# Performance work log

Measured on AMD Instinct MI355X. Metric: run time of the kernel, lower is better.

## Reference

```python
import jax, jax.numpy as jnp
import numpy as np

LN_EPS = 1e-5


def setup_inputs() -> dict:
    key = jax.random.key(0)
    ks = jax.random.split(key, 5)
    N, E, D = 50000, 600000, 128
    x = jax.random.normal(ks[0], (N, D), dtype=jnp.float32)
    edge_index = jax.random.randint(ks[1], (2, E), 0, N, dtype=jnp.int64)
    W_l = jax.random.normal(ks[2], (D, D), dtype=jnp.float32) * (1.0 / np.sqrt(D))
    b_l = jnp.zeros((D,), dtype=jnp.float32)
    W_r = jax.random.normal(ks[3], (D, D), dtype=jnp.float32) * (1.0 / np.sqrt(D))
    gamma = jnp.ones((D,), dtype=jnp.float32)
    beta = jnp.zeros((D,), dtype=jnp.float32)
    return {"x": x, "edge_index": edge_index, "W_l": W_l, "b_l": b_l,
            "W_r": W_r, "gamma": gamma, "beta": beta}


def reference(x, edge_index, W_l, b_l, W_r, gamma, beta):
    # SAGEConv (mean aggregation): out = lin_l(mean_{j in N(i)} x_j) + lin_r(x_i)
    N = x.shape[0]
    src, dst = edge_index[0], edge_index[1]
    msg = x[src]                                                # (E, D) gather
    agg = jax.ops.segment_sum(msg, dst, num_segments=N)         # (N, D) scatter-add
    cnt = jax.ops.segment_sum(jnp.ones_like(dst, dtype=x.dtype), dst, num_segments=N)
    mean = agg / jnp.maximum(cnt, 1.0)[:, None]
    h = mean @ W_l.T + b_l + x @ W_r.T                          # (N, D)
    # LayerNorm over feature dim
    mu = jnp.mean(h, axis=-1, keepdims=True)
    var = jnp.mean(jnp.square(h - mu), axis=-1, keepdims=True)
    h = (h - mu) * jax.lax.rsqrt(var + LN_EPS) * gamma + beta
    # ReLU; Dropout is identity in eval mode
    return jax.nn.relu(h)
```

## Files before the change

### kernel.cpp

```cpp
#include <hip/hip_runtime.h>
#include <stdint.h>

#define DIM 128
#define LN_EPS 1e-5f
#define BROWS 32
#define BINB 256
#define NT1 1024
#define SCAP 6
#define NBKT_MAX 1600
#define LELLS 56
#define LOVF 64
#define OVFCAP 4096
#define ATS 264
#define PINIT ((int)0xAAAAAAAA)

typedef __attribute__((ext_vector_type(8))) short bf16x8;
typedef __attribute__((ext_vector_type(4))) float f32x4;
typedef __attribute__((ext_vector_type(2))) float f32x2;
typedef __attribute__((ext_vector_type(4))) uint32_t u32x4;
typedef __attribute__((ext_vector_type(2))) uint32_t u32x2;

static __device__ __forceinline__ uint16_t f2bf(float f) {
    uint32_t u = __float_as_uint(f);
    return (uint16_t)((u + 0x7fffu + ((u >> 16) & 1u)) >> 16);
}
static __device__ __forceinline__ float bf_lo(uint32_t w) {
    return __uint_as_float(w << 16);
}
static __device__ __forceinline__ float bf_hi(uint32_t w) {
    return __uint_as_float(w & 0xffff0000u);
}

#define CONS(Q, PR, A) do { float _p = (PR); \
    A[0] = fmaf(_p, bf_lo(Q[0]), A[0]); A[1] = fmaf(_p, bf_hi(Q[0]), A[1]); \
    A[2] = fmaf(_p, bf_lo(Q[1]), A[2]); A[3] = fmaf(_p, bf_hi(Q[1]), A[3]); \
    A[4] = fmaf(_p, bf_lo(Q[2]), A[4]); A[5] = fmaf(_p, bf_hi(Q[2]), A[5]); \
    A[6] = fmaf(_p, bf_lo(Q[3]), A[6]); A[7] = fmaf(_p, bf_hi(Q[3]), A[7]); } while (0)

#define CONS8(Q, PS, A) do { float _s = (PS); uint32_t _w; \
    _w = Q.x; \
    A[0] = fmaf(_s, (float)(int8_t)(_w),       A[0]); \
    A[1] = fmaf(_s, (float)(int8_t)(_w >> 8),  A[1]); \
    A[2] = fmaf(_s, (float)(int8_t)(_w >> 16), A[2]); \
    A[3] = fmaf(_s, (float)(int8_t)(_w >> 24), A[3]); \
    _w = Q.y; \
    A[4] = fmaf(_s, (float)(int8_t)(_w),       A[4]); \
    A[5] = fmaf(_s, (float)(int8_t)(_w >> 8),  A[5]); \
    A[6] = fmaf(_s, (float)(int8_t)(_w >> 16), A[6]); \
    A[7] = fmaf(_s, (float)(int8_t)(_w >> 24), A[7]); } while (0)

__global__ __launch_bounds__(NT1) void bin_kernel(
    const int* __restrict__ ei,
    const float* __restrict__ x,
    const float* __restrict__ Wl,
    const float* __restrict__ Wr,
    uint8_t* __restrict__ cnt, uint32_t* __restrict__ bedge,
    int* __restrict__ novf, int* __restrict__ ovf,
    uint16_t* __restrict__ x16, uint8_t* __restrict__ x8,
    float* __restrict__ scales, uint16_t* __restrict__ wc,
    int E, int N, int nbkt)
{
    __shared__ int hist[NBKT_MAX];
    const int t = threadIdx.x, b = blockIdx.x;

    for (int i = t; i < nbkt; i += NT1) hist[i] = 0;
    __syncthreads();

    const int chunk = (E + BINB - 1) / BINB;
    const int e0 = b * chunk;
    const int e1 = (e0 + chunk < E) ? e0 + chunk : E;

    for (int e = e0 + t; e < e1; e += NT1)
        atomicAdd(&hist[ei[E + e] >> 5], 1);
    __syncthreads();

    for (int i = t; i < nbkt; i += NT1) {
        int c = hist[i];
        cnt[(size_t)i * BINB + b] = (uint8_t)(c > 255 ? 255 : c);
        hist[i] = 0;
    }
    __syncthreads();

    for (int e = e0 + t; e < e1; e += NT1) {
        int src = ei[e];
        int dst = ei[E + e];
        int bkt = dst >> 5;
        int r = atomicAdd(&hist[bkt], 1);
        if (r < SCAP) {
            bedge[((size_t)bkt * BINB + b) * SCAP + r] =
                ((uint32_t)(dst & 31) << 27) | (uint32_t)src;
        } else {
            int q = atomicAdd(novf, 1) - PINIT;
            if (q >= 0 && q < OVFCAP) { ovf[2 * q] = dst; ovf[2 * q + 1] = src; }
        }
    }

    {
        const int lane = t & 63;
        const int gw = (b * NT1 + t) >> 6;
        const int nw = (BINB * NT1) >> 6;
        for (int r = gw; r < N; r += nw) {
            f32x2 v = *(const f32x2*)(x + (size_t)r * DIM + 2 * lane);
            uint32_t u = ((uint32_t)f2bf(v.y) << 16) | (uint32_t)f2bf(v.x);
            ((uint32_t*)x16)[(size_t)r * 64 + lane] = u;
            float am = fmaxf(fabsf(v.x), fabsf(v.y));
            #pragma unroll
            for (int off = 1; off < 64; off <<= 1)
                am = fmaxf(am, __shfl_xor(am, off, 64));
            float inv = (am > 0.0f) ? (127.0f / am) : 0.0f;
            int q0 = (int)rintf(v.x * inv);
            int q1 = (int)rintf(v.y * inv);
            *(uint16_t*)(x8 + (size_t)r * DIM + 2 * lane) =
                (uint16_t)(((uint32_t)(q1 & 0xff) << 8) | (uint32_t)(q0 & 0xff));
            if (lane == 0) scales[r] = (am > 0.0f) ? (am / 127.0f) : 0.0f;
        }
    }

    {
        int tid = b * NT1 + t, nth = BINB * NT1;
        for (int i = tid; i < DIM * 256; i += nth) {
            int d = i >> 8, k = i & 255;
            float v = (k < DIM) ? Wl[d * DIM + k] : Wr[d * DIM + (k - DIM)];
            wc[i] = f2bf(v);
        }
    }
}

__global__ __launch_bounds__(256, 6) void fused_kernel(
    const uint16_t* __restrict__ x16,
    const uint8_t* __restrict__ x8,
    const float* __restrict__ scales,
    const uint8_t* __restrict__ cnt,
    const uint32_t* __restrict__ bedge,
    const int* __restrict__ novf,
    const int* __restrict__ ovf,
    const uint16_t* __restrict__ wc,
    const float* __restrict__ bl,
    const float* __restrict__ gma,
    const float* __restrict__ bta,
    float* __restrict__ out,
    int N, int E)
{
    __shared__ int ell_s[BROWS][LELLS];
    __shared__ int cnt_s[BROWS];
    __shared__ int lovf_s[LOVF];
    __shared__ int nlovf_s;
    __shared__ __align__(16) uint16_t atile[2][16 * ATS];
    __shared__ float pln[2][16][2][2];

    const int t    = threadIdx.x;
    const int lane = t & 63;
    const int w    = t >> 6;
    const int p    = w >> 1;
    const int h    = w & 1;
    const int tile_row0 = blockIdx.x * BROWS + p * 16;
    const int grow0     = tile_row0 + h * 8;
    const int lb        = p * 16 + h * 8;

    if (t < BROWS) cnt_s[t] = 0;
    if (t == BROWS) nlovf_s = 0;
    __syncthreads();

    {
        int c = cnt[(size_t)blockIdx.x * BINB + t];
        c = (c < SCAP) ? c : SCAP;
        const uint32_t* sp = bedge + ((size_t)blockIdx.x * BINB + t) * SCAP;
        for (int r = 0; r < c; ++r) {
            uint32_t pk = sp[r];
            int local = pk >> 27;
            int rr = atomicAdd(&cnt_s[local], 1);
            if (rr < LELLS) ell_s[local][rr] = (int)(pk & 0x07FFFFFF);
            else {
                int q = atomicAdd(&nlovf_s, 1);
                if (q < LOVF) lovf_s[q] = (int)pk;
            }
        }
    }
    __syncthreads();

    const int rr4 = lane >> 4;
    const int dq  = lane & 15;
    const int r0l = lb + rr4;
    const int r1l = lb + 4 + rr4;
    int dg0 = cnt_s[r0l];
    int dg1 = cnt_s[r1l];
    const int nl0 = dg0 < LELLS ? dg0 : LELLS;
    const int nl1 = dg1 < LELLS ? dg1 : LELLS;

    int mx = 0;
    #pragma unroll
    for (int r = 0; r < 8; ++r) {
        int d = __builtin_amdgcn_readfirstlane(cnt_s[lb + r]);
        int tt = d < LELLS ? d : LELLS;
        mx = (tt > mx) ? tt : mx;
    }

    float a0[8], a1[8];
    #pragma unroll
    for (int k = 0; k < 8; ++k) { a0[k] = 0.0f; a1[k] = 0.0f; }

    const uint64_t xq64 = (uint64_t)(uintptr_t)x8;
    const uint64_t sc64 = (uint64_t)(uintptr_t)scales;
    const int* rl0 = ell_s[r0l];
    const int* rl1 = ell_s[r1l];
    const uint32_t dqo8 = (uint32_t)dq * 8u;

    auto fet8 = [&](int jj, int nl, const int* rowlist) -> uint32_t {
        int slot = (jj < nl) ? jj : 0;
        uint32_t v = (uint32_t)rowlist[slot];
        return (jj < nl) ? ((v << 7) | dqo8) : dqo8;
    };
    auto fets = [&](int jj, int nl, const int* rowlist) -> uint32_t {
        int slot = (jj < nl) ? jj : 0;
        return ((uint32_t)rowlist[slot]) << 2;
    };

#define GLD2(dst, vo) \
    asm volatile("global_load_dwordx2 %0, %1, %2 sc0" \
                 : "=&v"(dst) : "v"(vo), "s"(xq64))
#define GLDS(dst, vo) \
    asm volatile("global_load_dword %0, %1, %2" \
                 : "=&v"(dst) : "v"(vo), "s"(sc64))
#define ISSUE(QG0, QG1, S0, S1, jj) do { \
    uint32_t _v0 = fet8(jj, nl0, rl0), _v1 = fet8(jj, nl1, rl1); \
    uint32_t _s0 = fets(jj, nl0, rl0), _s1 = fets(jj, nl1, rl1); \
    GLD2(QG0, _v0); GLD2(QG1, _v1); GLDS(S0, _s0); GLDS(S1, _s1); } while (0)
#define CONSUME(QG0, QG1, S0, S1, jj) do { \
    float _p0 = (jj < nl0) ? S0 : 0.0f; \
    float _p1 = (jj < nl1) ? S1 : 0.0f; \
    CONS8(QG0, _p0, a0); CONS8(QG1, _p1, a1); } while (0)

    u32x2 qA0, qA1, qB0, qB1, qC0, qC1;
    float sA0, sA1, sB0, sB1, sC0, sC1;
    if (mx > 0) {
        ISSUE(qA0, qA1, sA0, sA1, 0);
        ISSUE(qB0, qB1, sB0, sB1, 1);
        for (int j = 0; j < mx; j += 3) {
            ISSUE(qC0, qC1, sC0, sC1, j + 2);
            asm volatile("s_waitcnt vmcnt(8)" ::: "memory");
            __builtin_amdgcn_sched_barrier(0);
            CONSUME(qA0, qA1, sA0, sA1, j);
            ISSUE(qA0, qA1, sA0, sA1, j + 3);
            asm volatile("s_waitcnt vmcnt(8)" ::: "memory");
            __builtin_amdgcn_sched_barrier(0);
            if (j + 1 < mx) CONSUME(qB0, qB1, sB0, sB1, j + 1);
            ISSUE(qB0, qB1, sB0, sB1, j + 4);
            asm volatile("s_waitcnt vmcnt(8)" ::: "memory");
            __builtin_amdgcn_sched_barrier(0);
            if (j + 2 < mx) CONSUME(qC0, qC1, sC0, sC1, j + 2);
        }
        asm volatile("s_waitcnt vmcnt(0)" ::: "memory");
        __builtin_amdgcn_sched_barrier(0);
    }

    {
        int nl = __builtin_amdgcn_readfirstlane(nlovf_s);
        nl = (nl < 0) ? 0 : (nl > LOVF ? LOVF : nl);
        for (int i = 0; i < nl; ++i) {
            uint32_t pk = (uint32_t)lovf_s[i];
            int local = pk >> 27;
            if (local >= lb && local < lb + 8) {
                int srco = (int)(pk & 0x07FFFFFF);
                u32x4 qq = *(const u32x4*)(x16 + (size_t)srco * DIM + 8 * dq);
                CONS(qq, (local == r0l) ? 1.0f : 0.0f, a0);
                CONS(qq, (local == r1l) ? 1.0f : 0.0f, a1);
            }
        }
    }

    {
        int no = __builtin_amdgcn_readfirstlane(novf[0]) - PINIT;
        no = (no < 0) ? 0 : (no > OVFCAP ? OVFCAP : no);
        for (int base = 0; base < no; base += 64) {
            int i = base + lane;
            int dsto = -1, srco = 0;
            if (i < no) { dsto = ovf[2 * i]; srco = ovf[2 * i + 1]; }
            bool hit = (dsto >= grow0 && dsto < grow0 + 8);
            unsigned long long mb = __ballot(hit);
            while (mb) {
                int l = __ffsll(mb) - 1;
                mb &= mb - 1;
                int d2 = __shfl(dsto, l, 64);
                int s2 = __shfl(srco, l, 64);
                u32x4 qq = *(const u32x4*)(x16 + (size_t)s2 * DIM + 8 * dq);
                int h0 = (d2 == grow0 + rr4) ? 1 : 0;
                int h1 = (d2 == grow0 + 4 + rr4) ? 1 : 0;
                CONS(qq, h0 ? 1.0f : 0.0f, a0);
                CONS(qq, h1 ? 1.0f : 0.0f, a1);
                dg0 += h0; dg1 += h1;
            }
        }
    }

    {
        uint16_t* at = atile[p];
        float rc0 = (dg0 > 0) ? (1.0f / (float)dg0) : 0.0f;
        float rc1 = (dg1 > 0) ? (1.0f / (float)dg1) : 0.0f;
        int lr0 = h * 8 + rr4;
        int lr1 = h * 8 + 4 + rr4;
        u32x4 w0, w1;
        #pragma unroll
        for (int i = 0; i < 4; ++i) {
            w0[i] = ((uint32_t)f2bf(a0[2 * i + 1] * rc0) << 16) | f2bf(a0[2 * i] * rc0);
            w1[i] = ((uint32_t)f2bf(a1[2 * i + 1] * rc1) << 16) | f2bf(a1[2 * i] * rc1);
        }
        *(u32x4*)&at[lr0 * ATS + 8 * dq] = w0;
        *(u32x4*)&at[lr1 * ATS + 8 * dq] = w1;
        int row0g = grow0 + rr4;     int rs0 = (row0g < N) ? row0g : 0;
        int row1g = grow0 + 4 + rr4; int rs1 = (row1g < N) ? row1g : 0;
        u32x4 xv0 = *(const u32x4*)(x16 + (size_t)rs0 * DIM + 8 * dq);
        u32x4 xv1 = *(const u32x4*)(x16 + (size_t)rs1 * DIM + 8 * dq);
        *(u32x4*)&at[lr0 * ATS + 128 + 8 * dq] = xv0;
        *(u32x4*)&at[lr1 * ATS + 128 + 8 * dq] = xv1;
    }
    __syncthreads();

    const int nsub = lane & 15;
    const int quad = lane >> 4;
    const uint16_t* at = atile[p];

    f32x4 acc[4];
    #pragma unroll
    for (int tt = 0; tt < 4; ++tt) {
        float b = bl[(h * 4 + tt) * 16 + nsub];
        acc[tt] = (f32x4){b, b, b, b};
    }

    #pragma unroll
    for (int c = 0; c < 8; ++c) {
        bf16x8 af = *(const bf16x8*)&at[nsub * ATS + c * 32 + quad * 8];
        #pragma unroll
        for (int tt = 0; tt < 4; ++tt) {
            int tg = h * 4 + tt;
            bf16x8 bfr = *(const bf16x8*)&wc[(size_t)(tg * 16 + nsub) * 256 + c * 32 + quad * 8];
            acc[tt] = __builtin_amdgcn_mfma_f32_16x16x32_bf16(af, bfr, acc[tt], 0, 0, 0);
        }
    }

    #pragma unroll
    for (int i = 0; i < 4; ++i) {
        float s = 0.0f, q = 0.0f;
        #pragma unroll
        for (int tt = 0; tt < 4; ++tt) {
            float v = acc[tt][i];
            s += v;
            q += v * v;
        }
        #pragma unroll
        for (int off = 1; off < 16; off <<= 1) {
            s += __shfl_xor(s, off, 64);
            q += __shfl_xor(q, off, 64);
        }
        if (nsub == 0) {
            pln[p][quad * 4 + i][h][0] = s;
            pln[p][quad * 4 + i][h][1] = q;
        }
    }
    __syncthreads();

    #pragma unroll
    for (int i = 0; i < 4; ++i) {
        int lrow = quad * 4 + i;
        float s = pln[p][lrow][0][0] + pln[p][lrow][1][0];
        float q = pln[p][lrow][0][1] + pln[p][lrow][1][1];
        float mu = s * (1.0f / 128.0f);
        float var = q * (1.0f / 128.0f) - mu * mu;
        float rs = rsqrtf(fmaxf(var, 0.0f) + LN_EPS);
        int grow = tile_row0 + lrow;
        if (grow < N) {
            float* op = out + (size_t)grow * DIM;
            #pragma unroll
            for (int tt = 0; tt < 4; ++tt) {
                int f = (h * 4 + tt) * 16 + nsub;
                float o = fmaxf((acc[tt][i] - mu) * rs * gma[f] + bta[f], 0.0f);
                op[f] = o;
            }
        }
    }
}

extern "C" void kernel_launch(void* const* d_in, const int* in_sizes, int n_in,
                              void* d_out, int out_size, void* d_ws, size_t ws_size,
                              hipStream_t stream) {
    const float* x  = (const float*)d_in[0];
    const int* ei   = (const int*)d_in[1];
    const float* Wl = (const float*)d_in[2];
    const float* bl = (const float*)d_in[3];
    const float* Wr = (const float*)d_in[4];
    const float* ga = (const float*)d_in[5];
    const float* be = (const float*)d_in[6];
    float* out = (float*)d_out;

    int N = in_sizes[0] / DIM;
    int E = in_sizes[1] / 2;
    int nbkt = (N + BROWS - 1) / BROWS;

    uint8_t* cnt    = (uint8_t*)d_ws;
    int* novf       = (int*)(cnt + (size_t)nbkt * BINB);
    uint16_t* wc    = (uint16_t*)(novf + 16);
    uint16_t* x16   = wc + DIM * 256;
    float* scales   = (float*)(x16 + (size_t)N * DIM);
    uint8_t* x8     = (uint8_t*)(scales + N);
    uint32_t* bedge = (uint32_t*)(x8 + (size_t)N * DIM);
    int* ovf        = (int*)(bedge + (size_t)nbkt * BINB * SCAP);

    bin_kernel<<<BINB, NT1, 0, stream>>>(
        ei, x, Wl, Wr, cnt, bedge, novf, ovf, x16, x8, scales, wc, E, N, nbkt);

    fused_kernel<<<nbkt, 256, 0, stream>>>(
        x16, x8, scales, cnt, bedge, novf, ovf, wc, bl, ga, be, out, N, E);
}
```

Measured before the change: 153.6 us.

## Sort block rows by degree so each wave gathers similar-degree rows

Each block computes a rank permutation of its 32 destination rows by in-degree and assigns rows to waves in sorted order, so the 8 rows a wave handles have similar edge counts. The per-wave loop bound then comes from the largest degree in that group, which cuts wasted masked gather iterations caused by degree imbalance. Overflow handling is remapped through the inverse permutation, and results are written back to each row's original tile slot. The cost is an extra O(32^2) ranking step, an additional barrier, and a local-overflow path that now loads every entry instead of skipping non-matching rows.

```diff
diff --git a/kernel.cpp b/kernel.cpp
--- a/kernel.cpp
+++ b/kernel.cpp
@@ -143,6 +143,8 @@
 {
     __shared__ int ell_s[BROWS][LELLS];
     __shared__ int cnt_s[BROWS];
+    __shared__ int perm_s[BROWS];
+    __shared__ int inv_s[BROWS];
     __shared__ int lovf_s[LOVF];
     __shared__ int nlovf_s;
     __shared__ __align__(16) uint16_t atile[2][16 * ATS];
@@ -154,8 +156,7 @@
     const int p    = w >> 1;
     const int h    = w & 1;
     const int tile_row0 = blockIdx.x * BROWS + p * 16;
-    const int grow0     = tile_row0 + h * 8;
-    const int lb        = p * 16 + h * 8;
+    const int blockbase = blockIdx.x * BROWS;
 
     if (t < BROWS) cnt_s[t] = 0;
     if (t == BROWS) nlovf_s = 0;
@@ -178,22 +179,31 @@
     }
     __syncthreads();
 
+    if (t < BROWS) {
+        int ct = cnt_s[t];
+        int rank = 0;
+        for (int u = 0; u < BROWS; ++u) {
+            int cu = cnt_s[u];
+            rank += (cu < ct || (cu == ct && u < t)) ? 1 : 0;
+        }
+        perm_s[rank] = t;
+        inv_s[t] = rank;
+    }
+    __syncthreads();
+
     const int rr4 = lane >> 4;
     const int dq  = lane & 15;
-    const int r0l = lb + rr4;
-    const int r1l = lb + 4 + rr4;
-    int dg0 = cnt_s[r0l];
-    int dg1 = cnt_s[r1l];
+    const int l0  = perm_s[w * 8 + rr4];
+    const int l1  = perm_s[w * 8 + 4 + rr4];
+    const int g0  = blockbase + l0;
+    const int g1  = blockbase + l1;
+    int dg0 = cnt_s[l0];
+    int dg1 = cnt_s[l1];
     const int nl0 = dg0 < LELLS ? dg0 : LELLS;
     const int nl1 = dg1 < LELLS ? dg1 : LELLS;
 
-    int mx = 0;
-    #pragma unroll
-    for (int r = 0; r < 8; ++r) {
-        int d = __builtin_amdgcn_readfirstlane(cnt_s[lb + r]);
-        int tt = d < LELLS ? d : LELLS;
-        mx = (tt > mx) ? tt : mx;
-    }
+    int mx = __builtin_amdgcn_readfirstlane(cnt_s[perm_s[w * 8 + 7]]);
+    mx = mx < LELLS ? mx : LELLS;
 
     float a0[8], a1[8];
     #pragma unroll
@@ -201,8 +211,8 @@
 
     const uint64_t xq64 = (uint64_t)(uintptr_t)x8;
     const uint64_t sc64 = (uint64_t)(uintptr_t)scales;
-    const int* rl0 = ell_s[r0l];
-    const int* rl1 = ell_s[r1l];
+    const int* rl0 = ell_s[l0];
+    const int* rl1 = ell_s[l1];
     const uint32_t dqo8 = (uint32_t)dq * 8u;
 
     auto fet8 = [&](int jj, int nl, const int* rowlist) -> uint32_t {
@@ -258,13 +268,11 @@
         nl = (nl < 0) ? 0 : (nl > LOVF ? LOVF : nl);
         for (int i = 0; i < nl; ++i) {
             uint32_t pk = (uint32_t)lovf_s[i];
-            int local = pk >> 27;
-            if (local >= lb && local < lb + 8) {
-                int srco = (int)(pk & 0x07FFFFFF);
-                u32x4 qq = *(const u32x4*)(x16 + (size_t)srco * DIM + 8 * dq);
-                CONS(qq, (local == r0l) ? 1.0f : 0.0f, a0);
-                CONS(qq, (local == r1l) ? 1.0f : 0.0f, a1);
-            }
+            int local = (int)(pk >> 27);
+            int srco = (int)(pk & 0x07FFFFFF);
+            u32x4 qq = *(const u32x4*)(x16 + (size_t)srco * DIM + 8 * dq);
+            CONS(qq, (local == l0) ? 1.0f : 0.0f, a0);
+            CONS(qq, (local == l1) ? 1.0f : 0.0f, a1);
         }
     }
 
@@ -275,7 +283,10 @@
             int i = base + lane;
             int dsto = -1, srco = 0;
             if (i < no) { dsto = ovf[2 * i]; srco = ovf[2 * i + 1]; }
-            bool hit = (dsto >= grow0 && dsto < grow0 + 8);
+            int dl = dsto - blockbase;
+            bool inrange = (dl >= 0 && dl < BROWS);
+            int rk = inv_s[inrange ? dl : 0];
+            bool hit = inrange && ((rk >> 3) == w);
             unsigned long long mb = __ballot(hit);
             while (mb) {
                 int l = __ffsll(mb) - 1;
@@ -283,8 +294,8 @@
                 int d2 = __shfl(dsto, l, 64);
                 int s2 = __shfl(srco, l, 64);
                 u32x4 qq = *(const u32x4*)(x16 + (size_t)s2 * DIM + 8 * dq);
-                int h0 = (d2 == grow0 + rr4) ? 1 : 0;
-                int h1 = (d2 == grow0 + 4 + rr4) ? 1 : 0;
+                int h0 = (d2 == g0) ? 1 : 0;
+                int h1 = (d2 == g1) ? 1 : 0;
                 CONS(qq, h0 ? 1.0f : 0.0f, a0);
                 CONS(qq, h1 ? 1.0f : 0.0f, a1);
                 dg0 += h0; dg1 += h1;
@@ -293,25 +304,24 @@
     }
 
     {
-        uint16_t* at = atile[p];
         float rc0 = (dg0 > 0) ? (1.0f / (float)dg0) : 0.0f;
         float rc1 = (dg1 > 0) ? (1.0f / (float)dg1) : 0.0f;
-        int lr0 = h * 8 + rr4;
-        int lr1 = h * 8 + 4 + rr4;
         u32x4 w0, w1;
         #pragma unroll
         for (int i = 0; i < 4; ++i) {
             w0[i] = ((uint32_t)f2bf(a0[2 * i + 1] * rc0) << 16) | f2bf(a0[2 * i] * rc0);
             w1[i] = ((uint32_t)f2bf(a1[2 * i + 1] * rc1) << 16) | f2bf(a1[2 * i] * rc1);
         }
-        *(u32x4*)&at[lr0 * ATS + 8 * dq] = w0;
-        *(u32x4*)&at[lr1 * ATS + 8 * dq] = w1;
-        int row0g = grow0 + rr4;     int rs0 = (row0g < N) ? row0g : 0;
-        int row1g = grow0 + 4 + rr4; int rs1 = (row1g < N) ? row1g : 0;
+        int tp0 = l0 >> 4, lr0 = l0 & 15;
+        int tp1 = l1 >> 4, lr1 = l1 & 15;
+        *(u32x4*)&atile[tp0][lr0 * ATS + 8 * dq] = w0;
+        *(u32x4*)&atile[tp1][lr1 * ATS + 8 * dq] = w1;
+        int rs0 = (g0 < N) ? g0 : 0;
+        int rs1 = (g1 < N) ? g1 : 0;
         u32x4 xv0 = *(const u32x4*)(x16 + (size_t)rs0 * DIM + 8 * dq);
         u32x4 xv1 = *(const u32x4*)(x16 + (size_t)rs1 * DIM + 8 * dq);
-        *(u32x4*)&at[lr0 * ATS + 128 + 8 * dq] = xv0;
-        *(u32x4*)&at[lr1 * ATS + 128 + 8 * dq] = xv1;
+        *(u32x4*)&atile[tp0][lr0 * ATS + 128 + 8 * dq] = xv0;
+        *(u32x4*)&atile[tp1][lr1 * ATS + 128 + 8 * dq] = xv1;
     }
     __syncthreads();
 
```

Measured after the change: 161.2 us. 4.9% more time.
